# Kernel tuning notes

Measured on AMD Instinct MI355X. Metric: run time of the kernel, lower is better.

The kernel has to match this reference:

```python
import jax, jax.numpy as jnp
from jax import lax
import numpy as np
from functools import partial

B, N, T, H, L = 16, 256, 4, 128, 2
VOCAB, OUT_VOCAB, MAX_STEPS = 1000, 1000, 15


def setup_inputs() -> dict:
    key = jax.random.key(0)
    ks = jax.random.split(key, 13)
    data = jax.random.randint(ks[0], (B, N, T), 0, VOCAB)
    true_branch_nodes = jax.random.randint(ks[1], (B, N), 0, N)
    false_branch_nodes = jax.random.randint(ks[2], (B, N), 0, N)
    exit_index = jax.random.randint(ks[3], (B,), 0, N)
    steps = jax.random.randint(ks[4], (B,), 1, MAX_STEPS + 1)
    s_in = 1.0 / np.sqrt(H)
    s_cat = 1.0 / np.sqrt(2 * L * H)
    embed = jax.random.uniform(ks[5], (VOCAB, H), jnp.float32, -0.1, 0.1)
    Wi = jax.random.normal(ks[6], (L, H, 4 * H), jnp.float32) * s_in
    Wh = jax.random.normal(ks[7], (L, H, 4 * H), jnp.float32) * s_in
    b_lstm = jnp.zeros((L, 4 * H), jnp.float32)
    Wb = jax.random.normal(ks[8], (2 * L * H, 2), jnp.float32) * s_cat
    bb = jax.random.normal(ks[9], (2,), jnp.float32) * 1e-6
    Wo = jax.random.normal(ks[10], (2 * L * H, OUT_VOCAB), jnp.float32) * s_cat
    bo = jax.random.normal(ks[11], (OUT_VOCAB,), jnp.float32) * 1e-6
    return dict(data=data, true_branch_nodes=true_branch_nodes,
                false_branch_nodes=false_branch_nodes, exit_index=exit_index,
                steps=steps, embed=embed, Wi=Wi, Wh=Wh, b_lstm=b_lstm,
                Wb=Wb, bb=bb, Wo=Wo, bo=bo)


def _lstm_step(Wi_l, Wh_l, b_l, c, h, x):
    # flax LSTMCell math: gates from input (no bias) + recurrent (bias)
    z = x @ Wi_l + h @ Wh_l + b_l  # [..., 4H]
    i, f, g, o = jnp.split(z, 4, axis=-1)
    c2 = jax.nn.sigmoid(f) * c + jax.nn.sigmoid(i) * jnp.tanh(g)
    h2 = jax.nn.sigmoid(o) * jnp.tanh(c2)
    return c2, h2


def _forward(data, true_branch_nodes, false_branch_nodes, exit_index, steps,
             embed, Wi, Wh, b_lstm, Wb, bb, Wo, bo):
    emb = embed[data]                       # [B, N, T, H]
    cs = jnp.zeros((L, B, N, H), embed.dtype)
    hs = jnp.zeros((L, B, N, H), embed.dtype)
    ip = jnp.zeros((B, N), embed.dtype).at[:, 0].set(1.0)
    b_idx = jnp.arange(B)

    seg_b = jax.vmap(partial(jax.ops.segment_sum, num_segments=N))        # [B,N,...] , [B,N]
    seg_lb = jax.vmap(seg_b, in_axes=(0, None))                           # [L,B,N,H]

    def execute(cs, hs):
        # run the stacked LSTM over the T statement tokens at every node
        def tok_step(carry, x_t):
            cs, hs = carry
            inp = x_t
            nc, nh = [], []
            for l in range(L):
                c2, h2 = _lstm_step(Wi[l], Wh[l], b_lstm[l], cs[l], hs[l], inp)
                nc.append(c2); nh.append(h2)
                inp = h2
            return (jnp.stack(nc), jnp.stack(nh)), None
        (cs, hs), _ = lax.scan(tok_step, (cs, hs), jnp.moveaxis(emb, 2, 0))
        return cs, hs

    def step(carry, _):
        cs, hs, ip, idx = carry
        cs_c, hs_c = execute(cs, hs)
        # exit node keeps its previous hidden state
        cs_c = cs_c.at[:, b_idx, exit_index].set(cs[:, b_idx, exit_index])
        hs_c = hs_c.at[:, b_idx, exit_index].set(hs[:, b_idx, exit_index])
        # branch decision from concatenated (c, h) of every layer: [B, N, 2LH]
        feats = jnp.concatenate([x for l in range(L) for x in (cs_c[l], hs_c[l])], axis=-1)
        branch = jax.nn.softmax(feats @ Wb + bb, axis=-1)
        wt = branch[..., 0] * ip            # [B, N]
        wf = branch[..., 1] * ip
        ip_new = seg_b(wt, true_branch_nodes) + seg_b(wf, false_branch_nodes)
        denom = (ip_new + 1e-7)[None, :, :, None]
        def agg(h):
            return (seg_lb(h * wt[None, :, :, None], true_branch_nodes)
                    + seg_lb(h * wf[None, :, :, None], false_branch_nodes)) / denom
        cs_new, hs_new = agg(cs_c), agg(hs_c)
        live = idx < steps                   # [B]
        cs = jnp.where(live[None, :, None, None], cs_new, cs)
        hs = jnp.where(live[None, :, None, None], hs_new, hs)
        ip = jnp.where(live[:, None], ip_new, ip)
        return (cs, hs, ip, idx + 1), None

    (cs, hs, ip, _), _ = lax.scan(step, (cs, hs, ip, jnp.zeros((), jnp.int32)),
                                  None, length=MAX_STEPS)
    fc = cs[:, b_idx, exit_index]           # [L, B, H]
    fh = hs[:, b_idx, exit_index]
    final = jnp.concatenate([x for l in range(L) for x in (fc[l], fh[l])], axis=-1)
    logits = final @ Wo + bo                # [B, OUT_VOCAB]
    return logits[:, None, :]


def reference(data, true_branch_nodes, false_branch_nodes, exit_index, steps,
              embed, Wi, Wh, b_lstm, Wb, bb, Wo, bo):
    return _forward(data, true_branch_nodes, false_branch_nodes, exit_index,
                    steps, embed, Wi, Wh, b_lstm, Wb, bb, Wo, bo)
```

## Files before the change

kernel.cpp:

```cpp
#include <hip/hip_runtime.h>
#include <hip/hip_bf16.h>
#include <stdint.h>
#include <stddef.h>

static constexpr int BB = 16, NN = 256, TT = 4, HH = 128;
static constexpr int MM = BB * NN;
static constexpr int CC = 512;
static constexpr int OUTV = 1000;
static constexpr int MAXS = 15;
static constexpr int SP = 132;

typedef float f32x4 __attribute__((ext_vector_type(4)));
typedef short s16x8 __attribute__((ext_vector_type(8)));

__device__ __forceinline__ float sigf(float x) { return 1.0f / (1.0f + __expf(-x)); }
__device__ __forceinline__ float tanhr(float x) { return 2.0f / (1.0f + __expf(-2.0f * x)) - 1.0f; }
__device__ __forceinline__ unsigned short f2bu(float a) {
  return __builtin_bit_cast(unsigned short, __float2bfloat16(a));
}


__global__ void init_kernel(float* __restrict__ S, float* __restrict__ ip, int* __restrict__ count) {
  int tid = blockIdx.x * blockDim.x + threadIdx.x;
  int stride = gridDim.x * blockDim.x;
  int total = 4 * MM * HH;
  for (int i = tid; i < total; i += stride) S[i] = 0.0f;
  for (int i = tid; i < MM; i += stride) {
    ip[i] = ((i & (NN - 1)) == 0) ? 1.0f : 0.0f;
    count[i] = 0;
  }
}

__global__ void swz_kernel(const float* __restrict__ W, unsigned short* __restrict__ out) {
  int i = blockIdx.x * 256 + threadIdx.x;
  int j = i & 7, ln = (i >> 3) & 63, kb = (i >> 9) & 3, ct = i >> 11;
  int n = ln & 15, q = ln >> 4;
  int k = kb * 32 + q * 8 + j;
  int col = ct * 16 + n;
  out[i] = f2bu(W[k * CC + col]);
}

__global__ void xw0tab_kernel(const float* __restrict__ embed, const float* __restrict__ Wi0,
                              const float* __restrict__ b0, float* __restrict__ tab) {
  const int v0 = blockIdx.x * 8;
  const int j = threadIdx.x;
  __shared__ float A[8][HH];
  for (int s = j; s < 8 * HH; s += 256) {
    int r = s >> 7, k = s & 127;
    int v = v0 + r; if (v >= OUTV) v = OUTV - 1;
    A[r][k] = embed[(size_t)v * HH + k];
  }
  __syncthreads();
  float za[8], zb[8];
  {
    float ba = b0[j], bbv = b0[j + 256];
#pragma unroll
    for (int r = 0; r < 8; ++r) { za[r] = ba; zb[r] = bbv; }
  }
#pragma unroll 4
  for (int k = 0; k < HH; ++k) {
    float wa = Wi0[k * CC + j], wb = Wi0[k * CC + j + 256];
#pragma unroll
    for (int r = 0; r < 8; ++r) { za[r] += A[r][k] * wa; zb[r] += A[r][k] * wb; }
  }
#pragma unroll
  for (int r = 0; r < 8; ++r) {
    tab[(size_t)(v0 + r) * CC + j] = za[r];
    tab[(size_t)(v0 + r) * CC + j + 256] = zb[r];
  }
}

__global__ void edge_count(const int* __restrict__ tb, const int* __restrict__ fb,
                           int* __restrict__ count) {
  int e = blockIdx.x * blockDim.x + threadIdx.x;
  if (e >= 2 * MM) return;
  int b = e >> 9, r = e & 511, n = r >> 1, bit = r & 1;
  int tgt = bit ? fb[b * NN + n] : tb[b * NN + n];
  atomicAdd(&count[b * NN + tgt], 1);
}

__global__ void edge_scan(int* __restrict__ count, int* __restrict__ offs) {
  int b = blockIdx.x, tid = threadIdx.x;
  __shared__ int s[256];
  int v = count[b * NN + tid];
  s[tid] = v;
  __syncthreads();
  for (int off = 1; off < 256; off <<= 1) {
    int t = (tid >= off) ? s[tid - off] : 0;
    __syncthreads();
    s[tid] += t;
    __syncthreads();
  }
  offs[b * NN + tid] = b * 2 * NN + s[tid] - v;
  count[b * NN + tid] = 0;
  if (b == 0 && tid == 0) offs[MM] = 2 * MM;
}

__global__ void edge_fill(const int* __restrict__ tb, const int* __restrict__ fb,
                          const int* __restrict__ offs, int* __restrict__ cursor,
                          int* __restrict__ edges) {
  int e = blockIdx.x * blockDim.x + threadIdx.x;
  if (e >= 2 * MM) return;
  int b = e >> 9, r = e & 511, n = r >> 1, bit = r & 1;
  int tgt = bit ? fb[b * NN + n] : tb[b * NN + n];
  int pos = offs[b * NN + tgt] + atomicAdd(&cursor[b * NN + tgt], 1);
  edges[pos] = (n << 1) | bit;
}


__global__ __launch_bounds__(512, 2) void step_kernel(
    float* __restrict__ Sc0g, float* __restrict__ Sh0g,
    float* __restrict__ Sc1g, float* __restrict__ Sh1g,
    const float* __restrict__ Wr0, const float* __restrict__ Wr1,
    const float* __restrict__ Wr2, const float* __restrict__ Wr3,
    float* __restrict__ Ww0, float* __restrict__ Ww1,
    float* __restrict__ Ww2, float* __restrict__ Ww3,
    const float* __restrict__ wtR, const float* __restrict__ wfR,
    float* __restrict__ wtW, float* __restrict__ wfW,
    const float* __restrict__ ipg,
    const int* __restrict__ offs, const int* __restrict__ edges,
    const float* __restrict__ tab,
    const unsigned short* __restrict__ swzWh0, const unsigned short* __restrict__ swzWi1,
    const unsigned short* __restrict__ swzWh1, const float* __restrict__ b1,
    const float* __restrict__ Wb, const float* __restrict__ bb,
    const int* __restrict__ data, const int* __restrict__ exi,
    const int* __restrict__ steps, int step) {
  const int row0 = blockIdx.x * 16;
  const int b = row0 >> 8;
  const int sb = steps[b];
  const bool aggLive = (step >= 1) && ((step - 1) < sb);
  const bool lstmLive = (step < sb);
  if (!aggLive && !lstmLive) return;

  const int tid = threadIdx.x;
  const int w = tid >> 6;
  const int lane = tid & 63;
  const int n16 = lane & 15, qq = lane >> 4;
  const int kcol = w * 16 + n16;

  __shared__ float c0L[16 * SP], h0L[16 * SP], c1L[16 * SP], h1L[16 * SP];
  __shared__ __align__(16) unsigned short hA0[2048], hA1[2048];
  __shared__ float exitP[4][HH];
  __shared__ float ipL[16];
  __shared__ int toks[64];

  if (aggLive) {
    const int l = tid & 31;
    const int m = tid >> 5;
    const int node = row0 + m;
    int beg = offs[node], end = offs[node + 1];
    float a0x = 0.f, a0y = 0.f, a0z = 0.f, a0w = 0.f;
    float a1x = 0.f, a1y = 0.f, a1z = 0.f, a1w = 0.f;
    float a2x = 0.f, a2y = 0.f, a2z = 0.f, a2w = 0.f;
    float a3x = 0.f, a3y = 0.f, a3z = 0.f, a3w = 0.f;
    float wsum = 0.f;
    for (int e = beg; e < end; ++e) {
      int rec = edges[e];
      int src = (b << 8) + (rec >> 1);
      float wv = (rec & 1) ? wfR[src] : wtR[src];
      wsum += wv;
      float4 x0 = ((const float4*)Wr0)[src * 32 + l];
      float4 x1 = ((const float4*)Wr1)[src * 32 + l];
      float4 x2 = ((const float4*)Wr2)[src * 32 + l];
      float4 x3 = ((const float4*)Wr3)[src * 32 + l];
      a0x += wv * x0.x; a0y += wv * x0.y; a0z += wv * x0.z; a0w += wv * x0.w;
      a1x += wv * x1.x; a1y += wv * x1.y; a1z += wv * x1.z; a1w += wv * x1.w;
      a2x += wv * x2.x; a2y += wv * x2.y; a2z += wv * x2.z; a2w += wv * x2.w;
      a3x += wv * x3.x; a3y += wv * x3.y; a3z += wv * x3.z; a3w += wv * x3.w;
    }
    float inv = 1.0f / (wsum + 1e-7f);
    float4 o0 = { a0x * inv, a0y * inv, a0z * inv, a0w * inv };
    float4 o1 = { a1x * inv, a1y * inv, a1z * inv, a1w * inv };
    float4 o2 = { a2x * inv, a2y * inv, a2z * inv, a2w * inv };
    float4 o3 = { a3x * inv, a3y * inv, a3z * inv, a3w * inv };
    ((float4*)c0L)[m * (SP / 4) + l] = o0;
    ((float4*)h0L)[m * (SP / 4) + l] = o1;
    ((float4*)c1L)[m * (SP / 4) + l] = o2;
    ((float4*)h1L)[m * (SP / 4) + l] = o3;
    if (l == 0) ipL[m] = wsum;
    if (!lstmLive) {
      ((float4*)Sc0g)[node * 32 + l] = o0;
      ((float4*)Sh0g)[node * 32 + l] = o1;
      ((float4*)Sc1g)[node * 32 + l] = o2;
      ((float4*)Sh1g)[node * 32 + l] = o3;
    }
  } else {
    for (int s = tid; s < 16 * HH; s += 512) {
      int m = s >> 7, k = s & 127;
      size_t g = (size_t)(row0 + m) * HH + k;
      c0L[m * SP + k] = Sc0g[g];
      h0L[m * SP + k] = Sh0g[g];
      c1L[m * SP + k] = Sc1g[g];
      h1L[m * SP + k] = Sh1g[g];
    }
    if (tid < 16) ipL[tid] = ipg[row0 + tid];
  }
  if (!lstmLive) return;

  s16x8 B0[4][4], B1[4][4];
  const s16x8* pWh0 = (const s16x8*)swzWh0;
  const s16x8* pWh1 = (const s16x8*)swzWh1;
  const s16x8* pWi1 = (const s16x8*)swzWi1;
  float b1v[4];
#pragma unroll
  for (int g = 0; g < 4; ++g) {
    int ci = w + 8 * g;
#pragma unroll
    for (int kb = 0; kb < 4; ++kb) {
      B0[g][kb] = pWh0[(ci * 4 + kb) * 64 + lane];
      B1[g][kb] = pWh1[(ci * 4 + kb) * 64 + lane];
    }
    b1v[g] = b1[ci * 16 + n16];
  }

  const int exnode = exi[b];
  const int exm = exnode - (row0 & (NN - 1));
  if (tid < 64) toks[tid] = data[(row0 + (tid >> 2)) * TT + (tid & 3)];
  __syncthreads();

  if (exm >= 0 && exm < 16 && tid < 128) {
    exitP[0][tid] = c0L[exm * SP + tid];
    exitP[1][tid] = h0L[exm * SP + tid];
    exitP[2][tid] = c1L[exm * SP + tid];
    exitP[3][tid] = h1L[exm * SP + tid];
  }

  const int kb0 = kcol >> 5, q0 = (kcol >> 3) & 3, j0 = kcol & 7;
  const int basePos = (kb0 * 64 + q0 * 16) * 8 + j0;
  float c0r[4], c1r[4], h0r[4], h1r[4];
#pragma unroll
  for (int r = 0; r < 4; ++r) {
    int m = qq * 4 + r;
    c0r[r] = c0L[m * SP + kcol];
    c1r[r] = c1L[m * SP + kcol];
    h0r[r] = h0L[m * SP + kcol];
    h1r[r] = h1L[m * SP + kcol];
    hA0[basePos + m * 8] = f2bu(h0r[r]);
    hA1[basePos + m * 8] = f2bu(h1r[r]);
  }
  __syncthreads();

  const s16x8* hA0v = (const s16x8*)hA0;
  const s16x8* hA1v = (const s16x8*)hA1;

  for (int t = 0; t < TT; ++t) {
    s16x8 a0[4], a1b[4];
#pragma unroll
    for (int kb = 0; kb < 4; ++kb) { a0[kb] = hA0v[kb * 64 + lane]; a1b[kb] = hA1v[kb * 64 + lane]; }
    f32x4 d0[4];
#pragma unroll
    for (int g = 0; g < 4; ++g) {
      int colz = (w + 8 * g) * 16 + n16;
#pragma unroll
      for (int r = 0; r < 4; ++r)
        d0[g][r] = tab[(size_t)toks[(qq * 4 + r) * 4 + t] * CC + colz];
    }
    __syncthreads();

#pragma unroll
    for (int g = 0; g < 4; ++g)
#pragma unroll
      for (int kb = 0; kb < 4; ++kb)
        d0[g] = __builtin_amdgcn_mfma_f32_16x16x32_bf16(a0[kb], B0[g][kb], d0[g], 0, 0, 0);

#pragma unroll
    for (int r = 0; r < 4; ++r) {
      float cn = sigf(d0[1][r]) * c0r[r] + sigf(d0[0][r]) * tanhr(d0[2][r]);
      float hn = sigf(d0[3][r]) * tanhr(cn);
      c0r[r] = cn; h0r[r] = hn;
      hA0[basePos + (qq * 4 + r) * 8] = f2bu(hn);
    }
    __syncthreads();

    s16x8 a1a[4];
#pragma unroll
    for (int kb = 0; kb < 4; ++kb) a1a[kb] = hA0v[kb * 64 + lane];
    f32x4 d1[4];
#pragma unroll
    for (int g = 0; g < 4; ++g) {
      int ci = w + 8 * g;
      s16x8 wi[4];
#pragma unroll
      for (int kb = 0; kb < 4; ++kb) wi[kb] = pWi1[(ci * 4 + kb) * 64 + lane];
      f32x4 d = { b1v[g], b1v[g], b1v[g], b1v[g] };
#pragma unroll
      for (int kb = 0; kb < 4; ++kb)
        d = __builtin_amdgcn_mfma_f32_16x16x32_bf16(a1a[kb], wi[kb], d, 0, 0, 0);
#pragma unroll
      for (int kb = 0; kb < 4; ++kb)
        d = __builtin_amdgcn_mfma_f32_16x16x32_bf16(a1b[kb], B1[g][kb], d, 0, 0, 0);
      d1[g] = d;
    }

#pragma unroll
    for (int r = 0; r < 4; ++r) {
      float cn = sigf(d1[1][r]) * c1r[r] + sigf(d1[0][r]) * tanhr(d1[2][r]);
      float hn = sigf(d1[3][r]) * tanhr(cn);
      c1r[r] = cn; h1r[r] = hn;
      hA1[basePos + (qq * 4 + r) * 8] = f2bu(hn);
    }
    __syncthreads();
  }

#pragma unroll
  for (int r = 0; r < 4; ++r) {
    int m = qq * 4 + r;
    c0L[m * SP + kcol] = c0r[r];
    h0L[m * SP + kcol] = h0r[r];
    c1L[m * SP + kcol] = c1r[r];
    h1L[m * SP + kcol] = h1r[r];
  }
  __syncthreads();

  {
    const int m = tid >> 5, sub = tid & 31;
    const int row = row0 + m;
    const bool isExit = (m == exm);
    float z0 = 0.f, z1 = 0.f;
#pragma unroll
    for (int u = 0; u < 16; ++u) {
      int k = u * 32 + sub;
      int seg = k >> 7, kk = k & 127;
      float fk;
      if (isExit) {
        fk = exitP[seg][kk];
      } else {
        fk = (seg == 0) ? c0L[m * SP + kk] : (seg == 1) ? h0L[m * SP + kk]
           : (seg == 2) ? c1L[m * SP + kk] : h1L[m * SP + kk];
      }
      z0 += fk * Wb[2 * k];
      z1 += fk * Wb[2 * k + 1];
    }
#pragma unroll
    for (int off = 16; off >= 1; off >>= 1) {
      z0 += __shfl_xor(z0, off);
      z1 += __shfl_xor(z1, off);
    }
    if (sub == 0) {
      z0 += bb[0]; z1 += bb[1];
      float mx = fmaxf(z0, z1);
      float e0 = __expf(z0 - mx), e1 = __expf(z1 - mx);
      float inv = 1.0f / (e0 + e1);
      float ipv = ipL[m];
      wtW[row] = e0 * inv * ipv;
      wfW[row] = e1 * inv * ipv;
    }
  }

  for (int s = tid; s < 16 * HH; s += 512) {
    int m = s >> 7, k = s & 127;
    bool ex = (m == exm);
    size_t g = (size_t)(row0 + m) * HH + k;
    Ww0[g] = ex ? exitP[0][k] : c0L[m * SP + k];
    Ww1[g] = ex ? exitP[1][k] : h0L[m * SP + k];
    Ww2[g] = ex ? exitP[2][k] : c1L[m * SP + k];
    Ww3[g] = ex ? exitP[3][k] : h1L[m * SP + k];
  }
}

__global__ void final_kernel(const float* __restrict__ Sc0, const float* __restrict__ Sh0,
                             const float* __restrict__ Sc1, const float* __restrict__ Sh1,
                             const int* __restrict__ exi, const float* __restrict__ Wo,
                             const float* __restrict__ bo, float* __restrict__ out) {
  const int b = blockIdx.x >> 2;
  const int vt = blockIdx.x & 3;
  const int tid = threadIdx.x;
  __shared__ float f[512];
  int row = b * NN + exi[b];
  if (tid < 128) {
    size_t g = (size_t)row * HH + tid;
    f[tid] = Sc0[g];
    f[128 + tid] = Sh0[g];
    f[256 + tid] = Sc1[g];
    f[384 + tid] = Sh1[g];
  }
  __syncthreads();
  if (tid < 250) {
    int v = vt * 250 + tid;
    float acc = bo[v];
#pragma unroll 8
    for (int k = 0; k < 512; ++k) acc += f[k] * Wo[(size_t)k * OUTV + v];
    out[b * OUTV + v] = acc;
  }
}

__global__ void zero_out_kernel(float* __restrict__ out, int n) {
  int i = blockIdx.x * blockDim.x + threadIdx.x;
  if (i < n) out[i] = 0.0f;
}


extern "C" void kernel_launch(void* const* d_in, const int* in_sizes, int n_in,
                              void* d_out, int out_size, void* d_ws, size_t ws_size,
                              hipStream_t stream) {
  const int* data = (const int*)d_in[0];
  const int* tb   = (const int*)d_in[1];
  const int* fb   = (const int*)d_in[2];
  const int* exi  = (const int*)d_in[3];
  const int* steps = (const int*)d_in[4];
  const float* embed = (const float*)d_in[5];
  const float* Wi = (const float*)d_in[6];
  const float* Wh = (const float*)d_in[7];
  const float* bl = (const float*)d_in[8];
  const float* Wb = (const float*)d_in[9];
  const float* bb = (const float*)d_in[10];
  const float* Wo = (const float*)d_in[11];
  const float* bo = (const float*)d_in[12];
  float* out = (float*)d_out;

  const float* Wi0 = Wi;
  const float* Wi1 = Wi + HH * CC;
  const float* Wh0 = Wh;
  const float* Wh1 = Wh + HH * CC;
  const float* b0 = bl;
  const float* b1 = bl + CC;

  float* ws = (float*)d_ws;
  size_t off = 0;
  float* tab = ws + off;  off += (size_t)1024 * CC;
  float* Sc0 = ws + off;  off += (size_t)MM * HH;
  float* Sh0 = ws + off;  off += (size_t)MM * HH;
  float* Sc1 = ws + off;  off += (size_t)MM * HH;
  float* Sh1 = ws + off;  off += (size_t)MM * HH;
  float* WA[4], *WB[4];
  for (int i = 0; i < 4; ++i) { WA[i] = ws + off; off += (size_t)MM * HH; }
  for (int i = 0; i < 4; ++i) { WB[i] = ws + off; off += (size_t)MM * HH; }
  unsigned short* swzWh0 = (unsigned short*)(ws + off); off += (size_t)HH * CC / 2;
  unsigned short* swzWi1 = (unsigned short*)(ws + off); off += (size_t)HH * CC / 2;
  unsigned short* swzWh1 = (unsigned short*)(ws + off); off += (size_t)HH * CC / 2;
  float* ip = ws + off;   off += MM;
  float* wtA = ws + off;  off += MM;
  float* wfA = ws + off;  off += MM;
  float* wtB = ws + off;  off += MM;
  float* wfB = ws + off;  off += MM;
  int* count = (int*)(ws + off); off += MM;
  int* offs  = (int*)(ws + off); off += MM + 16;
  int* edges = (int*)(ws + off); off += 2 * MM;
  (void)in_sizes; (void)n_in; (void)out_size;

  if (ws_size < off * sizeof(float)) {
    zero_out_kernel<<<(BB * OUTV + 255) / 256, 256, 0, stream>>>(out, BB * OUTV);
    return;
  }

  init_kernel<<<256, 256, 0, stream>>>(Sc0, ip, count);
  swz_kernel<<<256, 256, 0, stream>>>(Wh0, swzWh0);
  swz_kernel<<<256, 256, 0, stream>>>(Wi1, swzWi1);
  swz_kernel<<<256, 256, 0, stream>>>(Wh1, swzWh1);
  xw0tab_kernel<<<128, 256, 0, stream>>>(embed, Wi0, b0, tab);
  edge_count<<<(2 * MM + 255) / 256, 256, 0, stream>>>(tb, fb, count);
  edge_scan<<<BB, 256, 0, stream>>>(count, offs);
  edge_fill<<<(2 * MM + 255) / 256, 256, 0, stream>>>(tb, fb, offs, count, edges);

  for (int s = 0; s <= MAXS; ++s) {
    float** Wwr = (s & 1) ? WB : WA;
    float** Wrd = (s & 1) ? WA : WB;
    float* wtWp = (s & 1) ? wtB : wtA;
    float* wfWp = (s & 1) ? wfB : wfA;
    float* wtRp = (s & 1) ? wtA : wtB;
    float* wfRp = (s & 1) ? wfA : wfB;
    step_kernel<<<MM / 16, 512, 0, stream>>>(
        Sc0, Sh0, Sc1, Sh1,
        Wrd[0], Wrd[1], Wrd[2], Wrd[3],
        Wwr[0], Wwr[1], Wwr[2], Wwr[3],
        wtRp, wfRp, wtWp, wfWp, ip,
        offs, edges, tab, swzWh0, swzWi1, swzWh1, b1, Wb, bb,
        data, exi, steps, s);
  }
  final_kernel<<<BB * 4, 256, 0, stream>>>(Sc0, Sh0, Sc1, Sh1, exi, Wo, bo, out);
}
```

Before: 596.4 us.

## Store inter-step LSTM state as packed bf16 and drop state zero-init

The per-step state exchange buffers move from four fp32 arrays to one interleaved bf16-packed array, so each source row is read with two 16-byte loads during edge aggregation instead of four. The goal is to halve the scatter/gather traffic between step kernels. The global state zeroing in init is removed, and step 0 now synthesizes zeros and the initial instruction pointer in shared memory. The three swizzle kernels are merged into one launch. Rounding the carried state to bf16 each step adds precision loss that accumulates over steps.

```diff
diff --git a/kernel.cpp b/kernel.cpp
--- a/kernel.cpp
+++ b/kernel.cpp
@@ -18,26 +18,26 @@
 __device__ __forceinline__ unsigned short f2bu(float a) {
   return __builtin_bit_cast(unsigned short, __float2bfloat16(a));
 }
-
-
-__global__ void init_kernel(float* __restrict__ S, float* __restrict__ ip, int* __restrict__ count) {
-  int tid = blockIdx.x * blockDim.x + threadIdx.x;
-  int stride = gridDim.x * blockDim.x;
-  int total = 4 * MM * HH;
-  for (int i = tid; i < total; i += stride) S[i] = 0.0f;
-  for (int i = tid; i < MM; i += stride) {
-    ip[i] = ((i & (NN - 1)) == 0) ? 1.0f : 0.0f;
-    count[i] = 0;
-  }
-}
-
-__global__ void swz_kernel(const float* __restrict__ W, unsigned short* __restrict__ out) {
+__device__ __forceinline__ unsigned int packh(float a, float b) {
+  return (unsigned int)f2bu(a) | ((unsigned int)f2bu(b) << 16);
+}
+__device__ __forceinline__ float blo(unsigned int u) { return __builtin_bit_cast(float, u << 16); }
+__device__ __forceinline__ float bhi(unsigned int u) { return __builtin_bit_cast(float, u & 0xffff0000u); }
+
+
+__global__ void init_kernel(int* __restrict__ count) {
   int i = blockIdx.x * 256 + threadIdx.x;
-  int j = i & 7, ln = (i >> 3) & 63, kb = (i >> 9) & 3, ct = i >> 11;
+  if (i < MM) count[i] = 0;
+}
+
+__global__ void swz_all_kernel(const float* __restrict__ Wh0, const float* __restrict__ Wi1,
+                               const float* __restrict__ Wh1, unsigned short* __restrict__ swz) {
+  int i = blockIdx.x * 256 + threadIdx.x;
+  int mtx = i >> 16, ii = i & 65535;
+  const float* W = (mtx == 0) ? Wh0 : (mtx == 1) ? Wi1 : Wh1;
+  int j = ii & 7, ln = (ii >> 3) & 63, kb = (ii >> 9) & 3, ct = ii >> 11;
   int n = ln & 15, q = ln >> 4;
-  int k = kb * 32 + q * 8 + j;
-  int col = ct * 16 + n;
-  out[i] = f2bu(W[k * CC + col]);
+  swz[i] = f2bu(W[(kb * 32 + q * 8 + j) * CC + ct * 16 + n]);
 }
 
 __global__ void xw0tab_kernel(const float* __restrict__ embed, const float* __restrict__ Wi0,
@@ -111,13 +111,9 @@
 __global__ __launch_bounds__(512, 2) void step_kernel(
     float* __restrict__ Sc0g, float* __restrict__ Sh0g,
     float* __restrict__ Sc1g, float* __restrict__ Sh1g,
-    const float* __restrict__ Wr0, const float* __restrict__ Wr1,
-    const float* __restrict__ Wr2, const float* __restrict__ Wr3,
-    float* __restrict__ Ww0, float* __restrict__ Ww1,
-    float* __restrict__ Ww2, float* __restrict__ Ww3,
+    const unsigned int* __restrict__ Pr, unsigned int* __restrict__ Pw,
     const float* __restrict__ wtR, const float* __restrict__ wfR,
     float* __restrict__ wtW, float* __restrict__ wfW,
-    const float* __restrict__ ipg,
     const int* __restrict__ offs, const int* __restrict__ edges,
     const float* __restrict__ tab,
     const unsigned short* __restrict__ swzWh0, const unsigned short* __restrict__ swzWi1,
@@ -137,10 +133,11 @@
   const int lane = tid & 63;
   const int n16 = lane & 15, qq = lane >> 4;
   const int kcol = w * 16 + n16;
+  const int basePos = ((kcol >> 5) * 64 + ((kcol >> 3) & 3) * 16) * 8 + (kcol & 7);
 
   __shared__ float c0L[16 * SP], h0L[16 * SP], c1L[16 * SP], h1L[16 * SP];
   __shared__ __align__(16) unsigned short hA0[2048], hA1[2048];
-  __shared__ float exitP[4][HH];
+  __shared__ float exitP[512];
   __shared__ float ipL[16];
   __shared__ int toks[64];
 
@@ -148,31 +145,30 @@
     const int l = tid & 31;
     const int m = tid >> 5;
     const int node = row0 + m;
-    int beg = offs[node], end = offs[node + 1];
-    float a0x = 0.f, a0y = 0.f, a0z = 0.f, a0w = 0.f;
-    float a1x = 0.f, a1y = 0.f, a1z = 0.f, a1w = 0.f;
-    float a2x = 0.f, a2y = 0.f, a2z = 0.f, a2w = 0.f;
-    float a3x = 0.f, a3y = 0.f, a3z = 0.f, a3w = 0.f;
+    const int beg = offs[node], end = offs[node + 1];
+    float ac0[4] = {0,0,0,0}, ah0[4] = {0,0,0,0}, ac1[4] = {0,0,0,0}, ah1[4] = {0,0,0,0};
     float wsum = 0.f;
     for (int e = beg; e < end; ++e) {
       int rec = edges[e];
       int src = (b << 8) + (rec >> 1);
       float wv = (rec & 1) ? wfR[src] : wtR[src];
       wsum += wv;
-      float4 x0 = ((const float4*)Wr0)[src * 32 + l];
-      float4 x1 = ((const float4*)Wr1)[src * 32 + l];
-      float4 x2 = ((const float4*)Wr2)[src * 32 + l];
-      float4 x3 = ((const float4*)Wr3)[src * 32 + l];
-      a0x += wv * x0.x; a0y += wv * x0.y; a0z += wv * x0.z; a0w += wv * x0.w;
-      a1x += wv * x1.x; a1y += wv * x1.y; a1z += wv * x1.z; a1w += wv * x1.w;
-      a2x += wv * x2.x; a2y += wv * x2.y; a2z += wv * x2.z; a2w += wv * x2.w;
-      a3x += wv * x3.x; a3y += wv * x3.y; a3z += wv * x3.z; a3w += wv * x3.w;
+      const uint4* pr = (const uint4*)(Pr + (size_t)src * 256 + 8 * l);
+      uint4 u0 = pr[0], u1 = pr[1];
+      ac0[0] += wv * blo(u0.x); ac0[1] += wv * bhi(u0.x);
+      ac0[2] += wv * blo(u0.y); ac0[3] += wv * bhi(u0.y);
+      ah0[0] += wv * blo(u0.z); ah0[1] += wv * bhi(u0.z);
+      ah0[2] += wv * blo(u0.w); ah0[3] += wv * bhi(u0.w);
+      ac1[0] += wv * blo(u1.x); ac1[1] += wv * bhi(u1.x);
+      ac1[2] += wv * blo(u1.y); ac1[3] += wv * bhi(u1.y);
+      ah1[0] += wv * blo(u1.z); ah1[1] += wv * bhi(u1.z);
+      ah1[2] += wv * blo(u1.w); ah1[3] += wv * bhi(u1.w);
     }
     float inv = 1.0f / (wsum + 1e-7f);
-    float4 o0 = { a0x * inv, a0y * inv, a0z * inv, a0w * inv };
-    float4 o1 = { a1x * inv, a1y * inv, a1z * inv, a1w * inv };
-    float4 o2 = { a2x * inv, a2y * inv, a2z * inv, a2w * inv };
-    float4 o3 = { a3x * inv, a3y * inv, a3z * inv, a3w * inv };
+    float4 o0 = { ac0[0]*inv, ac0[1]*inv, ac0[2]*inv, ac0[3]*inv };
+    float4 o1 = { ah0[0]*inv, ah0[1]*inv, ah0[2]*inv, ah0[3]*inv };
+    float4 o2 = { ac1[0]*inv, ac1[1]*inv, ac1[2]*inv, ac1[3]*inv };
+    float4 o3 = { ah1[0]*inv, ah1[1]*inv, ah1[2]*inv, ah1[3]*inv };
     ((float4*)c0L)[m * (SP / 4) + l] = o0;
     ((float4*)h0L)[m * (SP / 4) + l] = o1;
     ((float4*)c1L)[m * (SP / 4) + l] = o2;
@@ -185,19 +181,16 @@
       ((float4*)Sh1g)[node * 32 + l] = o3;
     }
   } else {
-    for (int s = tid; s < 16 * HH; s += 512) {
-      int m = s >> 7, k = s & 127;
-      size_t g = (size_t)(row0 + m) * HH + k;
-      c0L[m * SP + k] = Sc0g[g];
-      h0L[m * SP + k] = Sh0g[g];
-      c1L[m * SP + k] = Sc1g[g];
-      h1L[m * SP + k] = Sh1g[g];
-    }
-    if (tid < 16) ipL[tid] = ipg[row0 + tid];
+    for (int i2 = tid; i2 < 16 * HH; i2 += 512) {
+      int m = i2 >> 7, k = i2 & 127;
+      c0L[m * SP + k] = 0.f; h0L[m * SP + k] = 0.f;
+      c1L[m * SP + k] = 0.f; h1L[m * SP + k] = 0.f;
+    }
+    if (tid < 16) ipL[tid] = (((row0 + tid) & (NN - 1)) == 0) ? 1.0f : 0.0f;
   }
   if (!lstmLive) return;
 
-  s16x8 B0[4][4], B1[4][4];
+  s16x8 B0f[4][4], B1f[4][4];
   const s16x8* pWh0 = (const s16x8*)swzWh0;
   const s16x8* pWh1 = (const s16x8*)swzWh1;
   const s16x8* pWi1 = (const s16x8*)swzWi1;
@@ -207,8 +200,8 @@
     int ci = w + 8 * g;
 #pragma unroll
     for (int kb = 0; kb < 4; ++kb) {
-      B0[g][kb] = pWh0[(ci * 4 + kb) * 64 + lane];
-      B1[g][kb] = pWh1[(ci * 4 + kb) * 64 + lane];
+      B0f[g][kb] = pWh0[(ci * 4 + kb) * 64 + lane];
+      B1f[g][kb] = pWh1[(ci * 4 + kb) * 64 + lane];
     }
     b1v[g] = b1[ci * 16 + n16];
   }
@@ -219,14 +212,12 @@
   __syncthreads();
 
   if (exm >= 0 && exm < 16 && tid < 128) {
-    exitP[0][tid] = c0L[exm * SP + tid];
-    exitP[1][tid] = h0L[exm * SP + tid];
-    exitP[2][tid] = c1L[exm * SP + tid];
-    exitP[3][tid] = h1L[exm * SP + tid];
-  }
-
-  const int kb0 = kcol >> 5, q0 = (kcol >> 3) & 3, j0 = kcol & 7;
-  const int basePos = (kb0 * 64 + q0 * 16) * 8 + j0;
+    exitP[tid] = c0L[exm * SP + tid];
+    exitP[128 + tid] = h0L[exm * SP + tid];
+    exitP[256 + tid] = c1L[exm * SP + tid];
+    exitP[384 + tid] = h1L[exm * SP + tid];
+  }
+
   float c0r[4], c1r[4], h0r[4], h1r[4];
 #pragma unroll
   for (int r = 0; r < 4; ++r) {
@@ -261,7 +252,7 @@
     for (int g = 0; g < 4; ++g)
 #pragma unroll
       for (int kb = 0; kb < 4; ++kb)
-        d0[g] = __builtin_amdgcn_mfma_f32_16x16x32_bf16(a0[kb], B0[g][kb], d0[g], 0, 0, 0);
+        d0[g] = __builtin_amdgcn_mfma_f32_16x16x32_bf16(a0[kb], B0f[g][kb], d0[g], 0, 0, 0);
 
 #pragma unroll
     for (int r = 0; r < 4; ++r) {
@@ -288,7 +279,7 @@
         d = __builtin_amdgcn_mfma_f32_16x16x32_bf16(a1a[kb], wi[kb], d, 0, 0, 0);
 #pragma unroll
       for (int kb = 0; kb < 4; ++kb)
-        d = __builtin_amdgcn_mfma_f32_16x16x32_bf16(a1b[kb], B1[g][kb], d, 0, 0, 0);
+        d = __builtin_amdgcn_mfma_f32_16x16x32_bf16(a1b[kb], B1f[g][kb], d, 0, 0, 0);
       d1[g] = d;
     }
 
@@ -323,7 +314,7 @@
       int seg = k >> 7, kk = k & 127;
       float fk;
       if (isExit) {
-        fk = exitP[seg][kk];
+        fk = exitP[seg * 128 + kk];
       } else {
         fk = (seg == 0) ? c0L[m * SP + kk] : (seg == 1) ? h0L[m * SP + kk]
            : (seg == 2) ? c1L[m * SP + kk] : h1L[m * SP + kk];
@@ -347,14 +338,25 @@
     }
   }
 
-  for (int s = tid; s < 16 * HH; s += 512) {
-    int m = s >> 7, k = s & 127;
-    bool ex = (m == exm);
-    size_t g = (size_t)(row0 + m) * HH + k;
-    Ww0[g] = ex ? exitP[0][k] : c0L[m * SP + k];
-    Ww1[g] = ex ? exitP[1][k] : h0L[m * SP + k];
-    Ww2[g] = ex ? exitP[2][k] : c1L[m * SP + k];
-    Ww3[g] = ex ? exitP[3][k] : h1L[m * SP + k];
+  {
+    const int m = tid >> 5, l = tid & 31;
+    const bool ex = (m == exm);
+    const int grow = row0 + m;
+    float f0[4], f1[4], f2[4], f3[4];
+#pragma unroll
+    for (int i = 0; i < 4; ++i) {
+      int k = 4 * l + i;
+      f0[i] = ex ? exitP[k] : c0L[m * SP + k];
+      f1[i] = ex ? exitP[128 + k] : h0L[m * SP + k];
+      f2[i] = ex ? exitP[256 + k] : c1L[m * SP + k];
+      f3[i] = ex ? exitP[384 + k] : h1L[m * SP + k];
+    }
+    uint4 o0 = { packh(f0[0], f0[1]), packh(f0[2], f0[3]),
+                 packh(f1[0], f1[1]), packh(f1[2], f1[3]) };
+    uint4 o1 = { packh(f2[0], f2[1]), packh(f2[2], f2[3]),
+                 packh(f3[0], f3[1]), packh(f3[2], f3[3]) };
+    uint4* pw = (uint4*)(Pw + (size_t)grow * 256 + 8 * l);
+    pw[0] = o0; pw[1] = o1;
   }
 }
 
@@ -422,13 +424,9 @@
   float* Sh0 = ws + off;  off += (size_t)MM * HH;
   float* Sc1 = ws + off;  off += (size_t)MM * HH;
   float* Sh1 = ws + off;  off += (size_t)MM * HH;
-  float* WA[4], *WB[4];
-  for (int i = 0; i < 4; ++i) { WA[i] = ws + off; off += (size_t)MM * HH; }
-  for (int i = 0; i < 4; ++i) { WB[i] = ws + off; off += (size_t)MM * HH; }
-  unsigned short* swzWh0 = (unsigned short*)(ws + off); off += (size_t)HH * CC / 2;
-  unsigned short* swzWi1 = (unsigned short*)(ws + off); off += (size_t)HH * CC / 2;
-  unsigned short* swzWh1 = (unsigned short*)(ws + off); off += (size_t)HH * CC / 2;
-  float* ip = ws + off;   off += MM;
+  unsigned int* PA = (unsigned int*)(ws + off); off += (size_t)MM * 256;
+  unsigned int* PB = (unsigned int*)(ws + off); off += (size_t)MM * 256;
+  unsigned short* swz = (unsigned short*)(ws + off); off += 3 * 32768;
   float* wtA = ws + off;  off += MM;
   float* wfA = ws + off;  off += MM;
   float* wtB = ws + off;  off += MM;
@@ -443,27 +441,27 @@
     return;
   }
 
-  init_kernel<<<256, 256, 0, stream>>>(Sc0, ip, count);
-  swz_kernel<<<256, 256, 0, stream>>>(Wh0, swzWh0);
-  swz_kernel<<<256, 256, 0, stream>>>(Wi1, swzWi1);
-  swz_kernel<<<256, 256, 0, stream>>>(Wh1, swzWh1);
+  unsigned short* swzWh0 = swz;
+  unsigned short* swzWi1 = swz + 65536;
+  unsigned short* swzWh1 = swz + 2 * 65536;
+
+  init_kernel<<<16, 256, 0, stream>>>(count);
+  swz_all_kernel<<<768, 256, 0, stream>>>(Wh0, Wi1, Wh1, swz);
   xw0tab_kernel<<<128, 256, 0, stream>>>(embed, Wi0, b0, tab);
-  edge_count<<<(2 * MM + 255) / 256, 256, 0, stream>>>(tb, fb, count);
+  edge_count<<<32, 256, 0, stream>>>(tb, fb, count);
   edge_scan<<<BB, 256, 0, stream>>>(count, offs);
-  edge_fill<<<(2 * MM + 255) / 256, 256, 0, stream>>>(tb, fb, offs, count, edges);
+  edge_fill<<<32, 256, 0, stream>>>(tb, fb, offs, count, edges);
 
   for (int s = 0; s <= MAXS; ++s) {
-    float** Wwr = (s & 1) ? WB : WA;
-    float** Wrd = (s & 1) ? WA : WB;
+    unsigned int* Pwp = (s & 1) ? PB : PA;
+    const unsigned int* Prp = (s & 1) ? PA : PB;
     float* wtWp = (s & 1) ? wtB : wtA;
     float* wfWp = (s & 1) ? wfB : wfA;
-    float* wtRp = (s & 1) ? wtA : wtB;
-    float* wfRp = (s & 1) ? wfA : wfB;
+    const float* wtRp = (s & 1) ? wtA : wtB;
+    const float* wfRp = (s & 1) ? wfA : wfB;
     step_kernel<<<MM / 16, 512, 0, stream>>>(
-        Sc0, Sh0, Sc1, Sh1,
-        Wrd[0], Wrd[1], Wrd[2], Wrd[3],
-        Wwr[0], Wwr[1], Wwr[2], Wwr[3],
-        wtRp, wfRp, wtWp, wfWp, ip,
+        Sc0, Sh0, Sc1, Sh1, Prp, Pwp,
+        wtRp, wfRp, wtWp, wfWp,
         offs, edges, tab, swzWh0, swzWi1, swzWh1, b1, Wb, bb,
         data, exi, steps, s);
   }
```

After: 578.4 us. 3.0% less time.
